# Optimization experiments

Measured on AMD Instinct MI355X. Metric: run time of the kernel, lower is better.

The kernel has to match this reference:

```python
import jax, jax.numpy as jnp
import numpy as np

N_NODES = 20000
N_EDGES = 100000
WIDTH = 64
KER_IN = 6
KER_HID = WIDTH // 4  # 16
DEPTH = 6


def setup_inputs() -> dict:
    key = jax.random.key(0)
    ks = jax.random.split(key, 12)
    s = lambda fan_in: 1.0 / np.sqrt(fan_in)
    return {
        "x": jax.random.normal(ks[0], (N_NODES, 1), dtype=jnp.float32),
        "edge_index": jax.random.randint(ks[1], (2, N_EDGES), 0, N_NODES, dtype=jnp.int32),
        "edge_attr": jax.random.uniform(ks[2], (N_EDGES, KER_IN), dtype=jnp.float32),
        "fc1_w": jax.random.normal(ks[3], (1, WIDTH), dtype=jnp.float32) * s(1),
        "fc1_b": jnp.zeros((WIDTH,), dtype=jnp.float32),
        "k1_w": jax.random.normal(ks[4], (KER_IN, KER_HID), dtype=jnp.float32) * s(KER_IN),
        "k1_b": jnp.zeros((KER_HID,), dtype=jnp.float32),
        "k2_w": jax.random.normal(ks[5], (KER_HID, WIDTH * WIDTH), dtype=jnp.float32) * s(KER_HID),
        "k2_b": jnp.zeros((WIDTH * WIDTH,), dtype=jnp.float32),
        "root_w": jax.random.normal(ks[6], (WIDTH, WIDTH), dtype=jnp.float32) * s(WIDTH),
        "conv_b": jnp.zeros((WIDTH,), dtype=jnp.float32),
        "fc2_w": jax.random.normal(ks[7], (WIDTH, 1), dtype=jnp.float32) * s(WIDTH),
        "fc2_b": jnp.zeros((1,), dtype=jnp.float32),
    }


def reference(x, edge_index, edge_attr, fc1_w, fc1_b, k1_w, k1_b, k2_w, k2_b,
              root_w, conv_b, fc2_w, fc2_b):
    src = edge_index[0]  # source nodes j
    dst = edge_index[1]  # target nodes i

    # fc1: lift node features [N,1] -> [N,W]
    h = x @ fc1_w + fc1_b

    # Edge-conditioned weight matrices via kernel MLP (edge_attr is layer-invariant,
    # so compute once and reuse for all DEPTH layers — identical math).
    ek = jax.nn.relu(edge_attr @ k1_w + k1_b)           # [E, W/4]
    W = (ek @ k2_w + k2_b).reshape(N_EDGES, WIDTH, WIDTH)  # [E, W, W]

    # mean aggregation denominator (in-degree, clamped to avoid div-by-zero)
    deg = jax.ops.segment_sum(jnp.ones((N_EDGES,), dtype=h.dtype), dst,
                              num_segments=N_NODES)
    denom = jnp.maximum(deg, 1.0)[:, None]               # [N,1]

    for _ in range(DEPTH):
        # per-edge matmul: msg_e = x_src[e] @ W_e
        msg = jnp.einsum('ei,eio->eo', h[src], W)        # [E, W]
        agg = jax.ops.segment_sum(msg, dst, num_segments=N_NODES) / denom
        h = jax.nn.relu(agg + h @ root_w + conv_b)       # NNConv root weight + bias, then outer ReLU

    return h @ fc2_w + fc2_b                              # [N, 1]
```

## Files before the change

### kernel.cpp

```cpp
#include <hip/hip_runtime.h>
#include <hip/hip_bf16.h>


#define NN 20000
#define NE 100000
#define WD 64
#define DEPTH 6
#define TM 15
#define LSTR 1092

typedef __attribute__((ext_vector_type(8))) short bf16x8;
typedef __attribute__((ext_vector_type(4))) float f32x4;

__device__ __forceinline__ unsigned short f2bf(float v) {
    union { float f; unsigned u; } x; x.f = v;
    unsigned r = x.u + 0x7fffu + ((x.u >> 16) & 1u);
    return (unsigned short)(r >> 16);
}
__device__ __forceinline__ float bf2f(unsigned short b) {
    union { unsigned u; float f; } x; x.u = ((unsigned)b) << 16;
    return x.f;
}

__global__ __launch_bounds__(256) void count_kernel(const int* __restrict__ ei,
                                                    int* __restrict__ outc,
                                                    int* __restrict__ inc)
{
    int e = blockIdx.x * 256 + threadIdx.x;
    if (e >= NE) return;
    atomicAdd(&outc[ei[e]], 1);
    atomicAdd(&inc[ei[NE + e]], 1);
}

__global__ __launch_bounds__(256) void scanA_kernel(const int* __restrict__ cnt,
                                                    int* __restrict__ partials)
{
    int b = blockIdx.x, t = threadIdx.x, lane = t & 63, w = t >> 6;
    int base = b * 1024 + t * 4;
    int s = 0;
#pragma unroll
    for (int i = 0; i < 4; ++i) {
        int idx = base + i;
        if (idx < 2 * NN) s += cnt[idx];
    }
#pragma unroll
    for (int off = 32; off > 0; off >>= 1) s += __shfl_down(s, off, 64);
    __shared__ int wsum[4];
    if (lane == 0) wsum[w] = s;
    __syncthreads();
    if (t == 0) partials[b] = wsum[0] + wsum[1] + wsum[2] + wsum[3];
}

__global__ __launch_bounds__(64) void scanB_kernel(const int* __restrict__ partials,
                                                   int* __restrict__ bases)
{
    int l = threadIdx.x;
    int p = (l < 40) ? partials[l] : 0;
    int v = p;
#pragma unroll
    for (int off = 1; off < 64; off <<= 1) {
        int u = __shfl_up(v, off, 64);
        if (l >= off) v += u;
    }
    if (l < 40) bases[l] = v - p;
}

__global__ __launch_bounds__(256) void scanC_kernel(const int* __restrict__ cnt,
                                                    const int* __restrict__ bases,
                                                    int* __restrict__ rps,
                                                    int* __restrict__ rpd,
                                                    float* __restrict__ invd)
{
    int b = blockIdx.x, t = threadIdx.x, lane = t & 63, w = t >> 6;
    int base = b * 1024 + t * 4;
    int v[4], s = 0;
#pragma unroll
    for (int i = 0; i < 4; ++i) {
        int idx = base + i;
        v[i] = (idx < 2 * NN) ? cnt[idx] : 0;
        s += v[i];
    }
    int tsum = s, sc = s;
#pragma unroll
    for (int off = 1; off < 64; off <<= 1) {
        int u = __shfl_up(sc, off, 64);
        if (lane >= off) sc += u;
    }
    __shared__ int wtot[4];
    if (lane == 63) wtot[w] = sc;
    __syncthreads();
    int wbase = 0;
    for (int j = 0; j < w; ++j) wbase += wtot[j];
    int run = bases[b] + wbase + sc - tsum;
#pragma unroll
    for (int i = 0; i < 4; ++i) {
        int idx = base + i;
        int e = run; run += v[i];
        if (idx < NN) {
            rps[idx] = e;
        } else if (idx < 2 * NN) {
            rpd[idx - NN] = e - NE;
            invd[idx - NN] = 1.0f / fmaxf((float)v[i], 1.0f);
        }
    }
    if (b == 0 && t == 0) { rps[NN] = NE; rpd[NN] = NE; }
}

__global__ __launch_bounds__(256) void ekfill_kernel(
    const int* __restrict__ ei, const float* __restrict__ ea,
    const float* __restrict__ k1w, const float* __restrict__ k1b,
    const int* __restrict__ rps, const int* __restrict__ rpd,
    int* __restrict__ fs, int* __restrict__ fd,
    float* __restrict__ eks, int* __restrict__ ss2sd,
    int* __restrict__ slot2src)
{
    int e = blockIdx.x * 256 + threadIdx.x;
    if (e >= NE) return;
    int s = ei[e], d = ei[NE + e];
    float a[6];
#pragma unroll
    for (int i = 0; i < 6; ++i) a[i] = ea[e * 6 + i];
    int slot_s = rps[s] + atomicAdd(&fs[s], 1);
    int slot_d = rpd[d] + atomicAdd(&fd[d], 1);
    ss2sd[slot_s] = slot_d;
    slot2src[slot_s] = s;
#pragma unroll
    for (int j = 0; j < 16; ++j) {
        float v = k1b[j];
#pragma unroll
        for (int i = 0; i < 6; ++i) v = fmaf(a[i], k1w[i * 16 + j], v);
        eks[(size_t)slot_s * 16 + j] = fmaxf(v, 0.f);
    }
}

__global__ __launch_bounds__(256) void gwt_kernel(
    const float* __restrict__ k2w, const float* __restrict__ k2b,
    const float* __restrict__ rootw,
    unsigned short* __restrict__ Gh, unsigned short* __restrict__ Gl)
{
    int idx = blockIdx.x * 256 + threadIdx.x;
    if (idx >= 1152 * 64) return;
    int n = idx >> 6, k = idx & 63;
    int b = n >> 6, o = n & 63;
    float g;
    if (b < 16)       g = k2w[b * 4096 + k * 64 + o];
    else if (b == 16) g = k2b[k * 64 + o];
    else              g = rootw[k * 64 + o];
    unsigned short hi = f2bf(g);
    Gh[idx] = hi;
    Gl[idx] = f2bf(g - bf2f(hi));
}

__global__ __launch_bounds__(256) void h0_kernel(
    const float* __restrict__ x, const float* __restrict__ w,
    const float* __restrict__ b,
    unsigned short* __restrict__ hhi, unsigned short* __restrict__ hlo)
{
    int idx = blockIdx.x * 256 + threadIdx.x;
    if (idx >= NN * WD) return;
    int n = idx >> 6, o = idx & 63;
    float v = fmaf(x[n], w[o], b[o]);
    unsigned short hi = f2bf(v);
    hhi[idx] = hi;
    hlo[idx] = f2bf(v - bf2f(hi));
}

__global__ __launch_bounds__(512) void fused_kernel(
    const unsigned short* __restrict__ hhi, const unsigned short* __restrict__ hlo,
    const unsigned short* __restrict__ Gh, const unsigned short* __restrict__ Gl,
    const float* __restrict__ eks, const int* __restrict__ ss2sd,
    const int* __restrict__ slot2src, const int* __restrict__ rps,
    float* __restrict__ Proot, float* __restrict__ msg)
{
    __shared__ __align__(16) float Pt[TM * LSTR];
    int n0 = blockIdx.x * TM;
    int w = threadIdx.x >> 6, l = threadIdx.x & 63;
    int quad = l >> 4, lr = l & 15;
    int arow = n0 + lr;
    if (arow > NN - 1) arow = NN - 1;
    const bf16x8* pah = (const bf16x8*)(hhi + (size_t)arow * 64 + quad * 8);
    const bf16x8* pal = (const bf16x8*)(hlo + (size_t)arow * 64 + quad * 8);
    bf16x8 ah0 = pah[0], ah1 = pah[4];
    bf16x8 al0 = pal[0], al1 = pal[4];

    for (int st = w; st < 18; st += 8) {
        f32x4 acc[4];
#pragma unroll
        for (int t = 0; t < 4; ++t) acc[t] = (f32x4){0.f, 0.f, 0.f, 0.f};
#pragma unroll
        for (int t = 0; t < 4; ++t) {
            int brow = st * 64 + t * 16 + lr;
            const bf16x8* pbh = (const bf16x8*)(Gh + (size_t)brow * 64 + quad * 8);
            const bf16x8* pbl = (const bf16x8*)(Gl + (size_t)brow * 64 + quad * 8);
            bf16x8 bh0 = pbh[0], bh1 = pbh[4];
            bf16x8 bl0 = pbl[0], bl1 = pbl[4];
            f32x4 a = acc[t];
            a = __builtin_amdgcn_mfma_f32_16x16x32_bf16(ah0, bh0, a, 0, 0, 0);
            a = __builtin_amdgcn_mfma_f32_16x16x32_bf16(ah0, bl0, a, 0, 0, 0);
            a = __builtin_amdgcn_mfma_f32_16x16x32_bf16(al0, bh0, a, 0, 0, 0);
            a = __builtin_amdgcn_mfma_f32_16x16x32_bf16(ah1, bh1, a, 0, 0, 0);
            a = __builtin_amdgcn_mfma_f32_16x16x32_bf16(ah1, bl1, a, 0, 0, 0);
            a = __builtin_amdgcn_mfma_f32_16x16x32_bf16(al1, bh1, a, 0, 0, 0);
            acc[t] = a;
        }
        if (st < 17) {
#pragma unroll
            for (int t = 0; t < 4; ++t)
#pragma unroll
                for (int r = 0; r < 4; ++r) {
                    int row = quad * 4 + r;
                    if (row < TM)
                        Pt[row * LSTR + st * 64 + t * 16 + lr] = acc[t][r];
                }
        } else {
#pragma unroll
            for (int t = 0; t < 4; ++t)
#pragma unroll
                for (int r = 0; r < 4; ++r) {
                    int row = quad * 4 + r;
                    int gn = n0 + row;
                    if (row < TM && gn < NN)
                        Proot[(size_t)gn * 64 + t * 16 + lr] = acc[t][r];
                }
        }
    }
    __syncthreads();

    int nend = n0 + TM; if (nend > NN) nend = NN;
    int r0 = rps[n0], r1 = rps[nend];
    for (int s = r0 + w; s < r1; s += 8) {
        int ln = slot2src[s] - n0;
        float ekv = eks[(size_t)s * 16 + (l & 15)];
        int ds = ss2sd[s];
        const float* Pr = &Pt[ln * LSTR];
        float m = Pr[16 * 64 + l];
#pragma unroll
        for (int k = 0; k < 16; ++k)
            m = fmaf(__shfl(ekv, k, 64), Pr[k * 64 + l], m);
        msg[(size_t)ds * 64 + l] = m;
    }
}

__global__ __launch_bounds__(256) void agg_kernel(
    const float* __restrict__ msg, const int* __restrict__ rpd,
    const float* __restrict__ invd, const float* __restrict__ Proot,
    const float* __restrict__ convb, float* __restrict__ h,
    unsigned short* __restrict__ hhi, unsigned short* __restrict__ hlo)
{
    int i = blockIdx.x * 4 + (threadIdx.x >> 6);
    if (i >= NN) return;
    int l = threadIdx.x & 63;
    int r0 = rpd[i], r1 = rpd[i + 1];
    float acc = 0.f;
    for (int s = r0; s < r1; ++s) acc += msg[(size_t)s * 64 + l];
    float v = fmaf(acc, invd[i], Proot[(size_t)i * 64 + l] + convb[l]);
    v = fmaxf(v, 0.f);
    int idx = i * 64 + l;
    h[idx] = v;
    unsigned short hi = f2bf(v);
    hhi[idx] = hi;
    hlo[idx] = f2bf(v - bf2f(hi));
}

__global__ __launch_bounds__(256) void out_kernel(
    const float* __restrict__ h, const float* __restrict__ fc2_w,
    const float* __restrict__ fc2_b, float* __restrict__ out)
{
    int wave = blockIdx.x * 4 + (threadIdx.x >> 6);
    int lane = threadIdx.x & 63;
    float v = h[(size_t)wave * 64 + lane] * fc2_w[lane];
#pragma unroll
    for (int off = 32; off > 0; off >>= 1) v += __shfl_down(v, off);
    if (lane == 0) out[wave] = v + fc2_b[0];
}

extern "C" void kernel_launch(void* const* d_in, const int* in_sizes, int n_in,
                              void* d_out, int out_size, void* d_ws, size_t ws_size,
                              hipStream_t stream)
{
    const float* x         = (const float*)d_in[0];
    const int*   ei        = (const int*)  d_in[1];
    const float* edge_attr = (const float*)d_in[2];
    const float* fc1_w     = (const float*)d_in[3];
    const float* fc1_b     = (const float*)d_in[4];
    const float* k1_w      = (const float*)d_in[5];
    const float* k1_b      = (const float*)d_in[6];
    const float* k2_w      = (const float*)d_in[7];
    const float* k2_b      = (const float*)d_in[8];
    const float* root_w    = (const float*)d_in[9];
    const float* conv_b    = (const float*)d_in[10];
    const float* fc2_w     = (const float*)d_in[11];
    const float* fc2_b     = (const float*)d_in[12];
    float* out = (float*)d_out;

    float* ws = (float*)d_ws;
    size_t off = 0;
    int* cnt   = (int*)(ws + off); off += 4 * NN;
    int* outc  = cnt;
    int* inc   = cnt + NN;
    int* fs    = cnt + 2 * NN;
    int* fd    = cnt + 3 * NN;
    int* rps   = (int*)(ws + off); off += 20004;
    int* rpd   = (int*)(ws + off); off += 20004;
    int* partials = (int*)(ws + off); off += 64;
    int* bases    = (int*)(ws + off); off += 64;
    int* ss2sd    = (int*)(ws + off); off += NE;
    int* slot2src = (int*)(ws + off); off += NE;
    float* invd  = ws + off; off += NN;
    float* eks   = ws + off; off += (size_t)NE * 16;
    unsigned short* Gh  = (unsigned short*)(ws + off); off += 36864;
    unsigned short* Gl  = (unsigned short*)(ws + off); off += 36864;
    unsigned short* hhi = (unsigned short*)(ws + off); off += (size_t)NN * 32;
    unsigned short* hlo = (unsigned short*)(ws + off); off += (size_t)NN * 32;
    float* h     = ws + off; off += (size_t)NN * WD;
    float* msg   = ws + off; off += (size_t)NE * WD;
    float* Proot = ws + off; off += (size_t)NN * WD;

    hipMemsetAsync(cnt, 0, 4 * NN * sizeof(int), stream);
    count_kernel<<<(NE + 255) / 256, 256, 0, stream>>>(ei, outc, inc);
    scanA_kernel<<<40, 256, 0, stream>>>(cnt, partials);
    scanB_kernel<<<1, 64, 0, stream>>>(partials, bases);
    scanC_kernel<<<40, 256, 0, stream>>>(cnt, bases, rps, rpd, invd);
    ekfill_kernel<<<(NE + 255) / 256, 256, 0, stream>>>(ei, edge_attr, k1_w, k1_b,
                                                        rps, rpd, fs, fd, eks,
                                                        ss2sd, slot2src);
    gwt_kernel<<<(1152 * 64 + 255) / 256, 256, 0, stream>>>(k2_w, k2_b, root_w, Gh, Gl);
    h0_kernel<<<(NN * WD + 255) / 256, 256, 0, stream>>>(x, fc1_w, fc1_b, hhi, hlo);

    int ntiles = (NN + TM - 1) / TM;
    for (int layer = 0; layer < DEPTH; ++layer) {
        fused_kernel<<<ntiles, 512, 0, stream>>>(hhi, hlo, Gh, Gl, eks, ss2sd,
                                                 slot2src, rps, Proot, msg);
        agg_kernel<<<(NN + 3) / 4, 256, 0, stream>>>(msg, rpd, invd, Proot,
                                                     conv_b, h, hhi, hlo);
    }

    out_kernel<<<NN / 4, 256, 0, stream>>>(h, fc2_w, fc2_b, out);
}
```

Baseline: 628.2 us.

## Give each wave a contiguous source-slot range and cache P rows in registers

The message phase of the fused kernel now gives each wave a contiguous chunk of source-sorted slots. It walks the block's row pointers, cached in shared memory, to find the source node instead of reading a slot2src array. The 17 P values for the current source node are held in registers and reloaded only when the node changes. Edge kernel coefficients are loaded as uniform vector loads rather than shuffles. The slot2src buffer is removed, and the aggregation loop is unrolled by four with independent accumulators to expose more memory-level parallelism.

```diff
diff --git a/kernel.cpp b/kernel.cpp
--- a/kernel.cpp
+++ b/kernel.cpp
@@ -111,8 +111,7 @@
     const float* __restrict__ k1w, const float* __restrict__ k1b,
     const int* __restrict__ rps, const int* __restrict__ rpd,
     int* __restrict__ fs, int* __restrict__ fd,
-    float* __restrict__ eks, int* __restrict__ ss2sd,
-    int* __restrict__ slot2src)
+    float* __restrict__ eks, int* __restrict__ ss2sd)
 {
     int e = blockIdx.x * 256 + threadIdx.x;
     if (e >= NE) return;
@@ -123,7 +122,6 @@
     int slot_s = rps[s] + atomicAdd(&fs[s], 1);
     int slot_d = rpd[d] + atomicAdd(&fd[d], 1);
     ss2sd[slot_s] = slot_d;
-    slot2src[slot_s] = s;
 #pragma unroll
     for (int j = 0; j < 16; ++j) {
         float v = k1b[j];
@@ -169,13 +167,18 @@
     const unsigned short* __restrict__ hhi, const unsigned short* __restrict__ hlo,
     const unsigned short* __restrict__ Gh, const unsigned short* __restrict__ Gl,
     const float* __restrict__ eks, const int* __restrict__ ss2sd,
-    const int* __restrict__ slot2src, const int* __restrict__ rps,
-    float* __restrict__ Proot, float* __restrict__ msg)
+    const int* __restrict__ rps, float* __restrict__ Proot,
+    float* __restrict__ msg)
 {
     __shared__ __align__(16) float Pt[TM * LSTR];
+    __shared__ int rb[TM + 1];
     int n0 = blockIdx.x * TM;
     int w = threadIdx.x >> 6, l = threadIdx.x & 63;
     int quad = l >> 4, lr = l & 15;
+    if (threadIdx.x < TM + 1) {
+        int gi = n0 + threadIdx.x;
+        rb[threadIdx.x] = rps[gi > NN ? NN : gi];
+    }
     int arow = n0 + lr;
     if (arow > NN - 1) arow = NN - 1;
     const bf16x8* pah = (const bf16x8*)(hhi + (size_t)arow * 64 + quad * 8);
@@ -227,17 +230,40 @@
     __syncthreads();
 
     int nend = n0 + TM; if (nend > NN) nend = NN;
-    int r0 = rps[n0], r1 = rps[nend];
-    for (int s = r0 + w; s < r1; s += 8) {
-        int ln = slot2src[s] - n0;
-        float ekv = eks[(size_t)s * 16 + (l & 15)];
-        int ds = ss2sd[s];
-        const float* Pr = &Pt[ln * LSTR];
-        float m = Pr[16 * 64 + l];
-#pragma unroll
-        for (int k = 0; k < 16; ++k)
-            m = fmaf(__shfl(ekv, k, 64), Pr[k * 64 + l], m);
-        msg[(size_t)ds * 64 + l] = m;
+    int r0 = rb[0], r1 = rb[nend - n0];
+    int total = r1 - r0;
+    if (total <= 0) return;
+    int per = (total + 7) >> 3;
+    int s0 = r0 + w * per;
+    int s1 = s0 + per; if (s1 > r1) s1 = r1;
+    int ln = 0;
+    float p[17];
+    bool need = true;
+    for (int s = s0; s < s1; ++s) {
+        while (s >= rb[ln + 1]) { ++ln; need = true; }
+        if (need) {
+            const float* Pr = &Pt[ln * LSTR];
+#pragma unroll
+            for (int k = 0; k < 17; ++k) p[k] = Pr[k * 64 + l];
+            need = false;
+        }
+        int su = __builtin_amdgcn_readfirstlane(s);
+        const float* er = eks + (size_t)su * 16;
+        f32x4 e0 = *(const f32x4*)(er);
+        f32x4 e1 = *(const f32x4*)(er + 4);
+        f32x4 e2 = *(const f32x4*)(er + 8);
+        f32x4 e3 = *(const f32x4*)(er + 12);
+        int ds = ss2sd[su];
+        float ma = p[16], mb = 0.f;
+        ma = fmaf(e0[0], p[0], ma);  mb = fmaf(e0[1], p[1], mb);
+        ma = fmaf(e0[2], p[2], ma);  mb = fmaf(e0[3], p[3], mb);
+        ma = fmaf(e1[0], p[4], ma);  mb = fmaf(e1[1], p[5], mb);
+        ma = fmaf(e1[2], p[6], ma);  mb = fmaf(e1[3], p[7], mb);
+        ma = fmaf(e2[0], p[8], ma);  mb = fmaf(e2[1], p[9], mb);
+        ma = fmaf(e2[2], p[10], ma); mb = fmaf(e2[3], p[11], mb);
+        ma = fmaf(e3[0], p[12], ma); mb = fmaf(e3[1], p[13], mb);
+        ma = fmaf(e3[2], p[14], ma); mb = fmaf(e3[3], p[15], mb);
+        msg[(size_t)ds * 64 + l] = ma + mb;
     }
 }
 
@@ -251,8 +277,16 @@
     if (i >= NN) return;
     int l = threadIdx.x & 63;
     int r0 = rpd[i], r1 = rpd[i + 1];
-    float acc = 0.f;
-    for (int s = r0; s < r1; ++s) acc += msg[(size_t)s * 64 + l];
+    float a0 = 0.f, a1 = 0.f, a2 = 0.f, a3 = 0.f;
+    int s = r0;
+    for (; s + 3 < r1; s += 4) {
+        a0 += msg[(size_t)s * 64 + l];
+        a1 += msg[(size_t)(s + 1) * 64 + l];
+        a2 += msg[(size_t)(s + 2) * 64 + l];
+        a3 += msg[(size_t)(s + 3) * 64 + l];
+    }
+    for (; s < r1; ++s) a0 += msg[(size_t)s * 64 + l];
+    float acc = (a0 + a1) + (a2 + a3);
     float v = fmaf(acc, invd[i], Proot[(size_t)i * 64 + l] + convb[l]);
     v = fmaxf(v, 0.f);
     int idx = i * 64 + l;
@@ -305,7 +339,6 @@
     int* partials = (int*)(ws + off); off += 64;
     int* bases    = (int*)(ws + off); off += 64;
     int* ss2sd    = (int*)(ws + off); off += NE;
-    int* slot2src = (int*)(ws + off); off += NE;
     float* invd  = ws + off; off += NN;
     float* eks   = ws + off; off += (size_t)NE * 16;
     unsigned short* Gh  = (unsigned short*)(ws + off); off += 36864;
@@ -322,15 +355,14 @@
     scanB_kernel<<<1, 64, 0, stream>>>(partials, bases);
     scanC_kernel<<<40, 256, 0, stream>>>(cnt, bases, rps, rpd, invd);
     ekfill_kernel<<<(NE + 255) / 256, 256, 0, stream>>>(ei, edge_attr, k1_w, k1_b,
-                                                        rps, rpd, fs, fd, eks,
-                                                        ss2sd, slot2src);
+                                                        rps, rpd, fs, fd, eks, ss2sd);
     gwt_kernel<<<(1152 * 64 + 255) / 256, 256, 0, stream>>>(k2_w, k2_b, root_w, Gh, Gl);
     h0_kernel<<<(NN * WD + 255) / 256, 256, 0, stream>>>(x, fc1_w, fc1_b, hhi, hlo);
 
     int ntiles = (NN + TM - 1) / TM;
     for (int layer = 0; layer < DEPTH; ++layer) {
         fused_kernel<<<ntiles, 512, 0, stream>>>(hhi, hlo, Gh, Gl, eks, ss2sd,
-                                                 slot2src, rps, Proot, msg);
+                                                 rps, Proot, msg);
         agg_kernel<<<(NN + 3) / 4, 256, 0, stream>>>(msg, rpd, invd, Proot,
                                                      conv_b, h, hhi, hlo);
     }
```

Result: faster. 561.8 us (-10.6%).
